# Performance work log

Hardware: AMD Instinct MI355X
Metric: run time of the kernel (lower is better)

The kernel has to match this reference:

```python
import jax, jax.numpy as jnp
import numpy as np

N_NODES = 50000
N_EDGES = 500000
HIDDEN = 128
HEADS = 8
HEAD_DIM = HIDDEN // HEADS


def setup_inputs() -> dict:
    key = jax.random.key(0)
    ks = jax.random.split(key, 20)

    def lin_w(k, fin, fout):
        return (jax.random.normal(k, (fin, fout), jnp.float32) / np.sqrt(fin)).astype(jnp.float32)

    inp = {
        "h": jax.random.normal(ks[0], (N_NODES, HIDDEN), jnp.float32),
        "x": jax.random.normal(ks[1], (N_NODES, 3), jnp.float32),
        "src": jax.random.randint(ks[2], (N_EDGES,), 0, N_NODES, jnp.int32),
        "dst": jax.random.randint(ks[3], (N_EDGES,), 0, N_NODES, jnp.int32),
        "distances": jax.random.uniform(ks[4], (N_EDGES,), jnp.float32),
        # linear layers stored as [in, out] (transposed vs torch nn.Linear)
        "Wq": lin_w(ks[5], HIDDEN, HIDDEN), "bq": jnp.zeros((HIDDEN,), jnp.float32),
        "Wk": lin_w(ks[6], HIDDEN, HIDDEN), "bk": jnp.zeros((HIDDEN,), jnp.float32),
        "Wv": lin_w(ks[7], HIDDEN, HIDDEN), "bv": jnp.zeros((HIDDEN,), jnp.float32),
        "Wo": lin_w(ks[8], HIDDEN, HIDDEN), "bo": jnp.zeros((HIDDEN,), jnp.float32),
        "Wd": lin_w(ks[9], 1, HEADS), "bd": jnp.zeros((HEADS,), jnp.float32),
        "Wg1": lin_w(ks[10], HIDDEN, HIDDEN), "bg1": jnp.zeros((HIDDEN,), jnp.float32),
        "Wg2": lin_w(ks[11], HIDDEN, 1), "bg2": jnp.zeros((1,), jnp.float32),
    }
    return inp


def reference(h, x, src, dst, distances,
              Wq, bq, Wk, bk, Wv, bv, Wo, bo, Wd, bd, Wg1, bg1, Wg2, bg2):
    n = h.shape[0]
    heads = Wd.shape[1]
    dh = Wq.shape[1] // heads

    q = (h @ Wq + bq).reshape(n, heads, dh)
    k = (h @ Wk + bk).reshape(n, heads, dh)
    v = (h @ Wv + bv).reshape(n, heads, dh)

    q_src = q[src]            # [E, heads, dh]
    k_dst = k[dst]
    v_dst = v[dst]

    logits = jnp.einsum('ehd,ehd->eh', q_src, k_dst) / jnp.sqrt(jnp.asarray(dh, h.dtype))
    bias = (distances * distances)[:, None] @ Wd + bd      # [E, heads]
    lg = logits - bias

    # segment softmax over edges grouped by src node
    m = jax.ops.segment_max(lg, src, num_segments=n)        # [N, heads]
    ex = jnp.exp(lg - m[src])
    s = jax.ops.segment_sum(ex, src, num_segments=n)
    w = ex / jnp.maximum(s[src], 1e-9)                      # [E, heads]

    h_upd = jax.ops.segment_sum(v_dst * w[:, :, None], src, num_segments=n)
    h_out = h + h_upd.reshape(n, heads * dh) @ Wo + bo

    w_mean = w.mean(axis=1)                                 # mean over heads -> [E]
    disp = jax.ops.segment_sum((x[dst] - x[src]) * w_mean[:, None], src, num_segments=n)

    gate = jnp.tanh(jax.nn.silu(h_out @ Wg1 + bg1) @ Wg2 + bg2)  # [N, 1]
    x_out = x + gate * disp
    return (h_out, x_out)
```

## Files before the change

### kernel.cpp

```cpp
#include <hip/hip_runtime.h>
#include <math.h>

#define N_NODES 50000
#define N_EDGES 500000
#define HIDDEN 128
#define HEADS 8
#define HEAD_DIM 16

typedef __attribute__((ext_vector_type(8))) short short8;
typedef __attribute__((ext_vector_type(4))) float floatx4;

#define OFF_Q       0u
#define OFF_KV      6400000u
#define OFF_HHI     12800000u
#define OFF_HLO     16000000u
#define OFF_DISP    19200000u
#define OFF_CNT     19350016u
#define OFF_ROWPTR  19400032u
#define OFF_CURSOR  19450048u
#define OFF_ESD     19500064u
#define OFF_WSPLIT  20500064u

static __device__ __forceinline__ unsigned short f2bf(float f) {
    unsigned u = __builtin_bit_cast(unsigned, f);
    unsigned r = (u + 0x7FFFu + ((u >> 16) & 1u)) >> 16;
    return (unsigned short)r;
}
static __device__ __forceinline__ float bf2f(unsigned short s) {
    return __builtin_bit_cast(float, (unsigned)s << 16);
}

__global__ void k_zero_int(int* __restrict__ p, int n) {
    int i = blockIdx.x * 256 + threadIdx.x;
    if (i < n) p[i] = 0;
}

__global__ void k_split_w(const float* __restrict__ Wq, const float* __restrict__ Wk,
                          const float* __restrict__ Wv, const float* __restrict__ Wo,
                          const float* __restrict__ Wg1, unsigned short* __restrict__ ws) {
    int t = blockIdx.x * 256 + threadIdx.x;
    int m = t >> 14, r = t & 16383;
    int k = r >> 7, n = r & 127;
    const float* W = (m == 0) ? Wq : (m == 1) ? Wk : (m == 2) ? Wv : (m == 3) ? Wo : Wg1;
    float x = W[k * 128 + n];
    int kc = k >> 5, kin = k & 31, quad = kin >> 3, j = kin & 7;
    int ct = n >> 4, nin = n & 15, lane = quad * 16 + nin;
    unsigned base = ((((unsigned)(m * 4 + kc) * 8 + ct) * 2) * 64 + lane) * 8 + j;
    unsigned short a = f2bf(x);
    ws[base] = a;
    ws[base + 512] = f2bf(x - bf2f(a));
}

__global__ __launch_bounds__(256) void k_qkv_mfma(
    const float* __restrict__ h, const unsigned short* __restrict__ wsp,
    const float* __restrict__ bq, const float* __restrict__ bk, const float* __restrict__ bv,
    float* __restrict__ q, unsigned* __restrict__ kvp) {
    const int wave = threadIdx.x >> 6, lane = threadIdx.x & 63;
    const int quad = lane >> 4, l15 = lane & 15;
    const int ct0 = wave * 2;
    const int row0 = blockIdx.x * 32;

    floatx4 acc[3][2][2];
#pragma unroll
    for (int m = 0; m < 3; ++m)
#pragma unroll
        for (int c = 0; c < 2; ++c)
#pragma unroll
            for (int r = 0; r < 2; ++r) acc[m][c][r] = (floatx4){0.f, 0.f, 0.f, 0.f};

#pragma unroll
    for (int kc = 0; kc < 4; ++kc) {
        short8 ah[2], al[2];
#pragma unroll
        for (int rt = 0; rt < 2; ++rt) {
            int row = row0 + rt * 16 + l15;
            if (row >= N_NODES) row = N_NODES - 1;
            const float* hp = h + (size_t)row * 128 + kc * 32 + quad * 8;
            float4 f0 = *(const float4*)(hp);
            float4 f1 = *(const float4*)(hp + 4);
            float fv[8] = {f0.x, f0.y, f0.z, f0.w, f1.x, f1.y, f1.z, f1.w};
#pragma unroll
            for (int j = 0; j < 8; ++j) {
                unsigned short hi = f2bf(fv[j]);
                ah[rt][j] = (short)hi;
                al[rt][j] = (short)f2bf(fv[j] - bf2f(hi));
            }
        }
#pragma unroll
        for (int m = 0; m < 3; ++m) {
#pragma unroll
            for (int ctl = 0; ctl < 2; ++ctl) {
                unsigned fb = ((((unsigned)(m * 4 + kc) * 8 + (ct0 + ctl)) * 2) * 64 + lane) * 8;
                short8 bh = *(const short8*)(wsp + fb);
                short8 bl = *(const short8*)(wsp + fb + 512);
#pragma unroll
                for (int rt = 0; rt < 2; ++rt) {
                    acc[m][ctl][rt] = __builtin_amdgcn_mfma_f32_16x16x32_bf16(
                        ah[rt], bh, acc[m][ctl][rt], 0, 0, 0);
                    acc[m][ctl][rt] = __builtin_amdgcn_mfma_f32_16x16x32_bf16(
                        ah[rt], bl, acc[m][ctl][rt], 0, 0, 0);
                    acc[m][ctl][rt] = __builtin_amdgcn_mfma_f32_16x16x32_bf16(
                        al[rt], bh, acc[m][ctl][rt], 0, 0, 0);
                }
            }
        }
    }

#pragma unroll
    for (int ctl = 0; ctl < 2; ++ctl) {
        int col = (ct0 + ctl) * 16 + l15;
        float bq_ = bq[col], bk_ = bk[col], bv_ = bv[col];
#pragma unroll
        for (int rt = 0; rt < 2; ++rt) {
#pragma unroll
            for (int reg = 0; reg < 4; ++reg) {
                int row = row0 + rt * 16 + quad * 4 + reg;
                if (row < N_NODES) {
                    q[(size_t)row * 128 + col] = acc[0][ctl][rt][reg] + bq_;
                    unsigned kb = f2bf(acc[1][ctl][rt][reg] + bk_);
                    unsigned vb = f2bf(acc[2][ctl][rt][reg] + bv_);
                    kvp[(size_t)row * 128 + col] = kb | (vb << 16);
                }
            }
        }
    }
}

__global__ void k_count(const int* __restrict__ src, int* __restrict__ cnt) {
    int e = blockIdx.x * 256 + threadIdx.x;
    if (e < N_EDGES) atomicAdd(&cnt[src[e]], 1);
}

__global__ __launch_bounds__(1024) void k_scan1(const int* __restrict__ cnt,
                                                int* __restrict__ loc,
                                                int* __restrict__ bsum, int n) {
    __shared__ int buf[1024];
    int t = threadIdx.x;
    int i = blockIdx.x * 1024 + t;
    int val = (i < n) ? cnt[i] : 0;
    buf[t] = val;
    __syncthreads();
    for (int off = 1; off < 1024; off <<= 1) {
        int a = (t >= off) ? buf[t - off] : 0;
        __syncthreads();
        buf[t] += a;
        __syncthreads();
    }
    if (i < n) loc[i] = buf[t];
    if (t == 1023) bsum[blockIdx.x] = buf[1023];
}

__global__ void k_scan2(int* __restrict__ bsum, int nb) {
    int t = threadIdx.x;
    int v = (t < nb) ? bsum[t] : 0;
    for (int off = 1; off < 64; off <<= 1) {
        int a = __shfl_up(v, off);
        if (t >= off) v += a;
    }
    if (t < nb) bsum[t] = v;
}

__global__ void k_scan3(const int* __restrict__ cnt, const int* __restrict__ loc,
                        const int* __restrict__ bsum,
                        int* __restrict__ rowptr, int* __restrict__ cursor, int n) {
    int i = blockIdx.x * 256 + threadIdx.x;
    if (i < n) {
        int off = (i >= 1024) ? bsum[(i >> 10) - 1] : 0;
        int incl = loc[i] + off;
        rowptr[i + 1] = incl;
        cursor[i] = incl - cnt[i];
    }
    if (i == 0) rowptr[0] = 0;
}

__global__ void k_scatter(const int* __restrict__ src, const int* __restrict__ dst,
                          const float* __restrict__ dist, int* __restrict__ cursor,
                          int2* __restrict__ esd) {
    int e = blockIdx.x * 256 + threadIdx.x;
    if (e < N_EDGES) {
        int pos = atomicAdd(&cursor[src[e]], 1);
        float dd = dist[e];
        esd[pos] = make_int2(dst[e], __float_as_int(dd * dd));
    }
}

__global__ __launch_bounds__(256) void k_edge_node(
    const float* __restrict__ q, const unsigned* __restrict__ kvp,
    const float* __restrict__ x,
    const int2* __restrict__ esd, const int* __restrict__ rowptr,
    const float* __restrict__ Wd, const float* __restrict__ bd,
    unsigned short* __restrict__ hupd_hi, unsigned short* __restrict__ hupd_lo,
    float* __restrict__ disp) {
    const int wave = threadIdx.x >> 6, lane = threadIdx.x & 63;
    const int node = blockIdx.x * 4 + wave;
    const int h = lane >> 3, sub = lane & 7;
    const int beg = rowptr[node], end = rowptr[node + 1];

    const float2 qv = *(const float2*)(q + (size_t)node * 128 + 2 * lane);
    const float wdh = Wd[h], bdh = bd[h];
    const bool dal = (sub < 3);
    float xs = dal ? x[node * 3 + sub] : 0.f;
    const unsigned colo = 2 * lane;

    float acc0 = 0.f, acc1 = 0.f, s_own = 0.f, da = 0.f;

    for (int cb = beg; cb < end; cb += 64) {
        int idx = cb + lane;
        int dvec = 0; float d2vec = 0.f;
        if (idx < end) {
            int2 ed = esd[idx];
            dvec = ed.x;
            d2vec = __int_as_float(ed.y);
        }
        int clen = min(64, end - cb);
        int i = 0;
        for (; i + 4 <= clen; i += 4) {
            int di[4]; float dd2[4]; uint2 kv2[4]; float xg[4];
#pragma unroll
            for (int j = 0; j < 4; ++j) {
                di[j]  = __shfl(dvec, i + j);
                dd2[j] = __shfl(d2vec, i + j);
            }
#pragma unroll
            for (int j = 0; j < 4; ++j)
                kv2[j] = *(const uint2*)(kvp + (unsigned)di[j] * 128u + colo);
#pragma unroll
            for (int j = 0; j < 4; ++j)
                xg[j] = dal ? x[(unsigned)di[j] * 3u + sub] : 0.f;
#pragma unroll
            for (int j = 0; j < 4; ++j) {
                float k0 = __builtin_bit_cast(float, kv2[j].x << 16);
                float v0 = __builtin_bit_cast(float, kv2[j].x & 0xFFFF0000u);
                float k1 = __builtin_bit_cast(float, kv2[j].y << 16);
                float v1 = __builtin_bit_cast(float, kv2[j].y & 0xFFFF0000u);
                float p = qv.x * k0 + qv.y * k1;
                p += __shfl_xor(p, 1);
                p += __shfl_xor(p, 2);
                p += __shfl_xor(p, 4);
                float w = __expf(p * 0.25f - (dd2[j] * wdh + bdh));
                s_own += w;
                acc0 += v0 * w;
                acc1 += v1 * w;
                da += (xg[j] - xs) * w;
            }
        }
        for (; i < clen; ++i) {
            int dij  = __shfl(dvec, i);
            float d2 = __shfl(d2vec, i);
            uint2 kv2 = *(const uint2*)(kvp + (unsigned)dij * 128u + colo);
            float xgj = dal ? x[(unsigned)dij * 3u + sub] : 0.f;
            float k0 = __builtin_bit_cast(float, kv2.x << 16);
            float v0 = __builtin_bit_cast(float, kv2.x & 0xFFFF0000u);
            float k1 = __builtin_bit_cast(float, kv2.y << 16);
            float v1 = __builtin_bit_cast(float, kv2.y & 0xFFFF0000u);
            float p = qv.x * k0 + qv.y * k1;
            p += __shfl_xor(p, 1);
            p += __shfl_xor(p, 2);
            p += __shfl_xor(p, 4);
            float w = __expf(p * 0.25f - (d2 * wdh + bdh));
            s_own += w;
            acc0 += v0 * w;
            acc1 += v1 * w;
            da += (xgj - xs) * w;
        }
    }

    float inva = 1.f / fmaxf(s_own, 1e-9f);
    float o0 = acc0 * inva, o1 = acc1 * inva;
    unsigned short h0 = f2bf(o0), h1 = f2bf(o1);
    unsigned short l0 = f2bf(o0 - bf2f(h0)), l1 = f2bf(o1 - bf2f(h1));
    ((unsigned*)hupd_hi)[(size_t)node * 64 + lane] = (unsigned)h0 | ((unsigned)h1 << 16);
    ((unsigned*)hupd_lo)[(size_t)node * 64 + lane] = (unsigned)l0 | ((unsigned)l1 << 16);

    da *= 0.125f * inva;
    da += __shfl_xor(da, 8);
    da += __shfl_xor(da, 16);
    da += __shfl_xor(da, 32);
    if (lane < 3) disp[node * 3 + lane] = da;
}

__global__ __launch_bounds__(256) void k_hout_gate(
    const float* __restrict__ h,
    const unsigned short* __restrict__ hupd_hi, const unsigned short* __restrict__ hupd_lo,
    const unsigned short* __restrict__ wsp,
    const float* __restrict__ bo, const float* __restrict__ bg1,
    const float* __restrict__ Wg2, const float* __restrict__ bg2,
    const float* __restrict__ x, const float* __restrict__ disp,
    float* __restrict__ hout, float* __restrict__ xout) {
    __shared__ float hb[4][16 * 132];
    const int wave = threadIdx.x >> 6, lane = threadIdx.x & 63;
    const int quad = lane >> 4, l15 = lane & 15;
    const int row0 = blockIdx.x * 64 + wave * 16;
    float* hbw = hb[wave];

    floatx4 acc[8];
#pragma unroll
    for (int c = 0; c < 8; ++c) acc[c] = (floatx4){0.f, 0.f, 0.f, 0.f};
#pragma unroll
    for (int kc = 0; kc < 4; ++kc) {
        int row = row0 + l15;
        if (row >= N_NODES) row = N_NODES - 1;
        size_t aoff = (size_t)row * 128 + kc * 32 + quad * 8;
        short8 ah = *(const short8*)(hupd_hi + aoff);
        short8 al = *(const short8*)(hupd_lo + aoff);
#pragma unroll
        for (int ct = 0; ct < 8; ++ct) {
            unsigned fb = ((((unsigned)(3 * 4 + kc) * 8 + ct) * 2) * 64 + lane) * 8;
            short8 bh = *(const short8*)(wsp + fb);
            short8 bl = *(const short8*)(wsp + fb + 512);
            acc[ct] = __builtin_amdgcn_mfma_f32_16x16x32_bf16(ah, bh, acc[ct], 0, 0, 0);
            acc[ct] = __builtin_amdgcn_mfma_f32_16x16x32_bf16(ah, bl, acc[ct], 0, 0, 0);
            acc[ct] = __builtin_amdgcn_mfma_f32_16x16x32_bf16(al, bh, acc[ct], 0, 0, 0);
        }
    }

#pragma unroll
    for (int ct = 0; ct < 8; ++ct) {
        int col = ct * 16 + l15;
        float bias = bo[col];
#pragma unroll
        for (int reg = 0; reg < 4; ++reg) {
            int row = row0 + quad * 4 + reg;
            float val = acc[ct][reg] + bias;
            if (row < N_NODES) {
                val += h[(size_t)row * 128 + col];
                hout[(size_t)row * 128 + col] = val;
            }
            hbw[(quad * 4 + reg) * 132 + col] = val;
        }
    }
    __asm__ volatile("s_waitcnt lgkmcnt(0)" ::: "memory");

    floatx4 acc2[8];
#pragma unroll
    for (int c = 0; c < 8; ++c) acc2[c] = (floatx4){0.f, 0.f, 0.f, 0.f};
#pragma unroll
    for (int kc = 0; kc < 4; ++kc) {
        const float* ap = hbw + l15 * 132 + kc * 32 + quad * 8;
        float4 f0 = *(const float4*)(ap);
        float4 f1 = *(const float4*)(ap + 4);
        float fv[8] = {f0.x, f0.y, f0.z, f0.w, f1.x, f1.y, f1.z, f1.w};
        short8 ah, al;
#pragma unroll
        for (int j = 0; j < 8; ++j) {
            unsigned short hi = f2bf(fv[j]);
            ah[j] = (short)hi;
            al[j] = (short)f2bf(fv[j] - bf2f(hi));
        }
#pragma unroll
        for (int ct = 0; ct < 8; ++ct) {
            unsigned fb = ((((unsigned)(4 * 4 + kc) * 8 + ct) * 2) * 64 + lane) * 8;
            short8 bh = *(const short8*)(wsp + fb);
            short8 bl = *(const short8*)(wsp + fb + 512);
            acc2[ct] = __builtin_amdgcn_mfma_f32_16x16x32_bf16(ah, bh, acc2[ct], 0, 0, 0);
            acc2[ct] = __builtin_amdgcn_mfma_f32_16x16x32_bf16(ah, bl, acc2[ct], 0, 0, 0);
            acc2[ct] = __builtin_amdgcn_mfma_f32_16x16x32_bf16(al, bh, acc2[ct], 0, 0, 0);
        }
    }

    float pr[4] = {0.f, 0.f, 0.f, 0.f};
#pragma unroll
    for (int ct = 0; ct < 8; ++ct) {
        int col = ct * 16 + l15;
        float b1 = bg1[col];
        float w2 = Wg2[col];
#pragma unroll
        for (int reg = 0; reg < 4; ++reg) {
            float z = acc2[ct][reg] + b1;
            pr[reg] += (z / (1.f + __expf(-z))) * w2;
        }
    }
#pragma unroll
    for (int off = 1; off < 16; off <<= 1) {
#pragma unroll
        for (int reg = 0; reg < 4; ++reg) pr[reg] += __shfl_xor(pr[reg], off);
    }
    if (l15 == 0) {
        float b2 = bg2[0];
#pragma unroll
        for (int reg = 0; reg < 4; ++reg) {
            int row = row0 + quad * 4 + reg;
            if (row < N_NODES) {
                float g = tanhf(pr[reg] + b2);
#pragma unroll
                for (int dd = 0; dd < 3; ++dd) {
                    int oo = row * 3 + dd;
                    xout[oo] = x[oo] + g * disp[oo];
                }
            }
        }
    }
}

extern "C" void kernel_launch(void* const* d_in, const int* in_sizes, int n_in,
                              void* d_out, int out_size, void* d_ws, size_t ws_size,
                              hipStream_t stream) {
    const float* h    = (const float*)d_in[0];
    const float* x    = (const float*)d_in[1];
    const int*   src  = (const int*)d_in[2];
    const int*   dst  = (const int*)d_in[3];
    const float* dist = (const float*)d_in[4];
    const float* Wq = (const float*)d_in[5];  const float* bq = (const float*)d_in[6];
    const float* Wk = (const float*)d_in[7];  const float* bk = (const float*)d_in[8];
    const float* Wv = (const float*)d_in[9];  const float* bv = (const float*)d_in[10];
    const float* Wo = (const float*)d_in[11]; const float* bo = (const float*)d_in[12];
    const float* Wd = (const float*)d_in[13]; const float* bd = (const float*)d_in[14];
    const float* Wg1 = (const float*)d_in[15]; const float* bg1 = (const float*)d_in[16];
    const float* Wg2 = (const float*)d_in[17]; const float* bg2 = (const float*)d_in[18];

    float* ws    = (float*)d_ws;
    float* q     = ws + OFF_Q;
    unsigned* kvp = (unsigned*)(ws + OFF_KV);
    float* disp  = ws + OFF_DISP;
    int* cnt     = (int*)(ws + OFF_CNT);
    int* rowptr  = (int*)(ws + OFF_ROWPTR);
    int* cursor  = (int*)(ws + OFF_CURSOR);
    int2* esd    = (int2*)(ws + OFF_ESD);
    unsigned short* wsp = (unsigned short*)(ws + OFF_WSPLIT);
    int* loc    = (int*)(ws + OFF_Q);
    int* bsum   = (int*)(ws + OFF_Q + 500000u);
    unsigned short* hupd_hi = (unsigned short*)(ws + OFF_HHI);
    unsigned short* hupd_lo = (unsigned short*)(ws + OFF_HLO);
    float* hout = (float*)d_out;
    float* xout = hout + (size_t)N_NODES * HIDDEN;

    const int nscan = (N_NODES + 1023) / 1024;

    k_split_w<<<320, 256, 0, stream>>>(Wq, Wk, Wv, Wo, Wg1, wsp);
    k_zero_int<<<(N_NODES + 255) / 256, 256, 0, stream>>>(cnt, N_NODES);
    k_count<<<(N_EDGES + 255) / 256, 256, 0, stream>>>(src, cnt);
    k_scan1<<<nscan, 1024, 0, stream>>>(cnt, loc, bsum, N_NODES);
    k_scan2<<<1, 64, 0, stream>>>(bsum, nscan);
    k_scan3<<<(N_NODES + 255) / 256, 256, 0, stream>>>(cnt, loc, bsum, rowptr, cursor, N_NODES);
    k_scatter<<<(N_EDGES + 255) / 256, 256, 0, stream>>>(src, dst, dist, cursor, esd);
    k_qkv_mfma<<<(N_NODES + 31) / 32, 256, 0, stream>>>(h, wsp, bq, bk, bv, q, kvp);
    k_edge_node<<<N_NODES / 4, 256, 0, stream>>>(q, kvp, x, esd, rowptr,
                                                 Wd, bd, hupd_hi, hupd_lo, disp);
    k_hout_gate<<<(N_NODES + 63) / 64, 256, 0, stream>>>(h, hupd_hi, hupd_lo, wsp,
                                                         bo, bg1, Wg2, bg2,
                                                         x, disp, hout, xout);
}
```

Before: 286.9 us.

## Merge small preprocessing kernels and co-launch QKV GEMM with edge scatter

Folds the weight split and count zeroing into one launch, merges the two scan fix-up kernels into one that redoes the tiny block-sum scan per block in shared memory, and packs the QKV MFMA GEMM and the CSR edge scatter into a single grid whose block ranges do different work. This cuts the kernel launch count from nine to six and lets the compute-bound GEMM blocks overlap with the atomic-bound scatter blocks. The cost is a heterogeneous grid, where the GEMM blocks' register use sets occupancy for the scatter blocks, plus redundant scan work in every scan23 block.

New measurement: 262.7 us. 1.09x faster.

```diff
diff --git a/kernel.cpp b/kernel.cpp
--- a/kernel.cpp
+++ b/kernel.cpp
@@ -6,6 +6,11 @@
 #define HIDDEN 128
 #define HEADS 8
 #define HEAD_DIM 16
+
+#define QKV_BLOCKS 1563
+#define SCAT_BLOCKS 1954
+#define SPLITW_BLOCKS 320
+#define ZERO_BLOCKS 196
 
 typedef __attribute__((ext_vector_type(8))) short short8;
 typedef __attribute__((ext_vector_type(4))) float floatx4;
@@ -30,14 +35,15 @@
     return __builtin_bit_cast(float, (unsigned)s << 16);
 }
 
-__global__ void k_zero_int(int* __restrict__ p, int n) {
-    int i = blockIdx.x * 256 + threadIdx.x;
-    if (i < n) p[i] = 0;
-}
-
-__global__ void k_split_w(const float* __restrict__ Wq, const float* __restrict__ Wk,
-                          const float* __restrict__ Wv, const float* __restrict__ Wo,
-                          const float* __restrict__ Wg1, unsigned short* __restrict__ ws) {
+__global__ void k_prep(const float* __restrict__ Wq, const float* __restrict__ Wk,
+                       const float* __restrict__ Wv, const float* __restrict__ Wo,
+                       const float* __restrict__ Wg1, unsigned short* __restrict__ ws,
+                       int* __restrict__ cnt) {
+    if (blockIdx.x >= SPLITW_BLOCKS) {
+        int i = (blockIdx.x - SPLITW_BLOCKS) * 256 + threadIdx.x;
+        if (i < N_NODES) cnt[i] = 0;
+        return;
+    }
     int t = blockIdx.x * 256 + threadIdx.x;
     int m = t >> 14, r = t & 16383;
     int k = r >> 7, n = r & 127;
@@ -49,81 +55,6 @@
     unsigned short a = f2bf(x);
     ws[base] = a;
     ws[base + 512] = f2bf(x - bf2f(a));
-}
-
-__global__ __launch_bounds__(256) void k_qkv_mfma(
-    const float* __restrict__ h, const unsigned short* __restrict__ wsp,
-    const float* __restrict__ bq, const float* __restrict__ bk, const float* __restrict__ bv,
-    float* __restrict__ q, unsigned* __restrict__ kvp) {
-    const int wave = threadIdx.x >> 6, lane = threadIdx.x & 63;
-    const int quad = lane >> 4, l15 = lane & 15;
-    const int ct0 = wave * 2;
-    const int row0 = blockIdx.x * 32;
-
-    floatx4 acc[3][2][2];
-#pragma unroll
-    for (int m = 0; m < 3; ++m)
-#pragma unroll
-        for (int c = 0; c < 2; ++c)
-#pragma unroll
-            for (int r = 0; r < 2; ++r) acc[m][c][r] = (floatx4){0.f, 0.f, 0.f, 0.f};
-
-#pragma unroll
-    for (int kc = 0; kc < 4; ++kc) {
-        short8 ah[2], al[2];
-#pragma unroll
-        for (int rt = 0; rt < 2; ++rt) {
-            int row = row0 + rt * 16 + l15;
-            if (row >= N_NODES) row = N_NODES - 1;
-            const float* hp = h + (size_t)row * 128 + kc * 32 + quad * 8;
-            float4 f0 = *(const float4*)(hp);
-            float4 f1 = *(const float4*)(hp + 4);
-            float fv[8] = {f0.x, f0.y, f0.z, f0.w, f1.x, f1.y, f1.z, f1.w};
-#pragma unroll
-            for (int j = 0; j < 8; ++j) {
-                unsigned short hi = f2bf(fv[j]);
-                ah[rt][j] = (short)hi;
-                al[rt][j] = (short)f2bf(fv[j] - bf2f(hi));
-            }
-        }
-#pragma unroll
-        for (int m = 0; m < 3; ++m) {
-#pragma unroll
-            for (int ctl = 0; ctl < 2; ++ctl) {
-                unsigned fb = ((((unsigned)(m * 4 + kc) * 8 + (ct0 + ctl)) * 2) * 64 + lane) * 8;
-                short8 bh = *(const short8*)(wsp + fb);
-                short8 bl = *(const short8*)(wsp + fb + 512);
-#pragma unroll
-                for (int rt = 0; rt < 2; ++rt) {
-                    acc[m][ctl][rt] = __builtin_amdgcn_mfma_f32_16x16x32_bf16(
-                        ah[rt], bh, acc[m][ctl][rt], 0, 0, 0);
-                    acc[m][ctl][rt] = __builtin_amdgcn_mfma_f32_16x16x32_bf16(
-                        ah[rt], bl, acc[m][ctl][rt], 0, 0, 0);
-                    acc[m][ctl][rt] = __builtin_amdgcn_mfma_f32_16x16x32_bf16(
-                        al[rt], bh, acc[m][ctl][rt], 0, 0, 0);
-                }
-            }
-        }
-    }
-
-#pragma unroll
-    for (int ctl = 0; ctl < 2; ++ctl) {
-        int col = (ct0 + ctl) * 16 + l15;
-        float bq_ = bq[col], bk_ = bk[col], bv_ = bv[col];
-#pragma unroll
-        for (int rt = 0; rt < 2; ++rt) {
-#pragma unroll
-            for (int reg = 0; reg < 4; ++reg) {
-                int row = row0 + rt * 16 + quad * 4 + reg;
-                if (row < N_NODES) {
-                    q[(size_t)row * 128 + col] = acc[0][ctl][rt][reg] + bq_;
-                    unsigned kb = f2bf(acc[1][ctl][rt][reg] + bk_);
-                    unsigned vb = f2bf(acc[2][ctl][rt][reg] + bv_);
-                    kvp[(size_t)row * 128 + col] = kb | (vb << 16);
-                }
-            }
-        }
-    }
 }
 
 __global__ void k_count(const int* __restrict__ src, int* __restrict__ cnt) {
@@ -150,22 +81,25 @@
     if (t == 1023) bsum[blockIdx.x] = buf[1023];
 }
 
-__global__ void k_scan2(int* __restrict__ bsum, int nb) {
+__global__ __launch_bounds__(256) void k_scan23(const int* __restrict__ cnt,
+                                                const int* __restrict__ loc,
+                                                const int* __restrict__ bsum,
+                                                int* __restrict__ rowptr,
+                                                int* __restrict__ cursor, int n, int nb) {
+    __shared__ int sb[64];
     int t = threadIdx.x;
-    int v = (t < nb) ? bsum[t] : 0;
-    for (int off = 1; off < 64; off <<= 1) {
-        int a = __shfl_up(v, off);
-        if (t >= off) v += a;
-    }
-    if (t < nb) bsum[t] = v;
-}
-
-__global__ void k_scan3(const int* __restrict__ cnt, const int* __restrict__ loc,
-                        const int* __restrict__ bsum,
-                        int* __restrict__ rowptr, int* __restrict__ cursor, int n) {
-    int i = blockIdx.x * 256 + threadIdx.x;
+    if (t < 64) {
+        int v = (t < nb) ? bsum[t] : 0;
+        for (int off = 1; off < 64; off <<= 1) {
+            int a = __shfl_up(v, off);
+            if (t >= off) v += a;
+        }
+        sb[t] = v;
+    }
+    __syncthreads();
+    int i = blockIdx.x * 256 + t;
     if (i < n) {
-        int off = (i >= 1024) ? bsum[(i >> 10) - 1] : 0;
+        int off = (i >= 1024) ? sb[(i >> 10) - 1] : 0;
         int incl = loc[i] + off;
         rowptr[i + 1] = incl;
         cursor[i] = incl - cnt[i];
@@ -173,14 +107,90 @@
     if (i == 0) rowptr[0] = 0;
 }
 
-__global__ void k_scatter(const int* __restrict__ src, const int* __restrict__ dst,
-                          const float* __restrict__ dist, int* __restrict__ cursor,
-                          int2* __restrict__ esd) {
-    int e = blockIdx.x * 256 + threadIdx.x;
-    if (e < N_EDGES) {
-        int pos = atomicAdd(&cursor[src[e]], 1);
-        float dd = dist[e];
-        esd[pos] = make_int2(dst[e], __float_as_int(dd * dd));
+__global__ __launch_bounds__(256) void k_qkv_scatter(
+    const float* __restrict__ h, const unsigned short* __restrict__ wsp,
+    const float* __restrict__ bq, const float* __restrict__ bk, const float* __restrict__ bv,
+    float* __restrict__ q, unsigned* __restrict__ kvp,
+    const int* __restrict__ src, const int* __restrict__ dst,
+    const float* __restrict__ dist, int* __restrict__ cursor, int2* __restrict__ esd) {
+    if (blockIdx.x >= QKV_BLOCKS) {
+        int e = (blockIdx.x - QKV_BLOCKS) * 256 + threadIdx.x;
+        if (e < N_EDGES) {
+            int pos = atomicAdd(&cursor[src[e]], 1);
+            float dd = dist[e];
+            esd[pos] = make_int2(dst[e], __float_as_int(dd * dd));
+        }
+        return;
+    }
+
+    const int wave = threadIdx.x >> 6, lane = threadIdx.x & 63;
+    const int quad = lane >> 4, l15 = lane & 15;
+    const int ct0 = wave * 2;
+    const int row0 = blockIdx.x * 32;
+
+    floatx4 acc[3][2][2];
+#pragma unroll
+    for (int m = 0; m < 3; ++m)
+#pragma unroll
+        for (int c = 0; c < 2; ++c)
+#pragma unroll
+            for (int r = 0; r < 2; ++r) acc[m][c][r] = (floatx4){0.f, 0.f, 0.f, 0.f};
+
+#pragma unroll
+    for (int kc = 0; kc < 4; ++kc) {
+        short8 ah[2], al[2];
+#pragma unroll
+        for (int rt = 0; rt < 2; ++rt) {
+            int row = row0 + rt * 16 + l15;
+            if (row >= N_NODES) row = N_NODES - 1;
+            const float* hp = h + (size_t)row * 128 + kc * 32 + quad * 8;
+            float4 f0 = *(const float4*)(hp);
+            float4 f1 = *(const float4*)(hp + 4);
+            float fv[8] = {f0.x, f0.y, f0.z, f0.w, f1.x, f1.y, f1.z, f1.w};
+#pragma unroll
+            for (int j = 0; j < 8; ++j) {
+                unsigned short hi = f2bf(fv[j]);
+                ah[rt][j] = (short)hi;
+                al[rt][j] = (short)f2bf(fv[j] - bf2f(hi));
+            }
+        }
+#pragma unroll
+        for (int m = 0; m < 3; ++m) {
+#pragma unroll
+            for (int ctl = 0; ctl < 2; ++ctl) {
+                unsigned fb = ((((unsigned)(m * 4 + kc) * 8 + (ct0 + ctl)) * 2) * 64 + lane) * 8;
+                short8 bh = *(const short8*)(wsp + fb);
+                short8 bl = *(const short8*)(wsp + fb + 512);
+#pragma unroll
+                for (int rt = 0; rt < 2; ++rt) {
+                    acc[m][ctl][rt] = __builtin_amdgcn_mfma_f32_16x16x32_bf16(
+                        ah[rt], bh, acc[m][ctl][rt], 0, 0, 0);
+                    acc[m][ctl][rt] = __builtin_amdgcn_mfma_f32_16x16x32_bf16(
+                        ah[rt], bl, acc[m][ctl][rt], 0, 0, 0);
+                    acc[m][ctl][rt] = __builtin_amdgcn_mfma_f32_16x16x32_bf16(
+                        al[rt], bh, acc[m][ctl][rt], 0, 0, 0);
+                }
+            }
+        }
+    }
+
+#pragma unroll
+    for (int ctl = 0; ctl < 2; ++ctl) {
+        int col = (ct0 + ctl) * 16 + l15;
+        float bq_ = bq[col], bk_ = bk[col], bv_ = bv[col];
+#pragma unroll
+        for (int rt = 0; rt < 2; ++rt) {
+#pragma unroll
+            for (int reg = 0; reg < 4; ++reg) {
+                int row = row0 + rt * 16 + quad * 4 + reg;
+                if (row < N_NODES) {
+                    q[(size_t)row * 128 + col] = acc[0][ctl][rt][reg] + bq_;
+                    unsigned kb = f2bf(acc[1][ctl][rt][reg] + bk_);
+                    unsigned vb = f2bf(acc[2][ctl][rt][reg] + bv_);
+                    kvp[(size_t)row * 128 + col] = kb | (vb << 16);
+                }
+            }
+        }
     }
 }
 
@@ -426,14 +436,12 @@
 
     const int nscan = (N_NODES + 1023) / 1024;
 
-    k_split_w<<<320, 256, 0, stream>>>(Wq, Wk, Wv, Wo, Wg1, wsp);
-    k_zero_int<<<(N_NODES + 255) / 256, 256, 0, stream>>>(cnt, N_NODES);
-    k_count<<<(N_EDGES + 255) / 256, 256, 0, stream>>>(src, cnt);
+    k_prep<<<SPLITW_BLOCKS + ZERO_BLOCKS, 256, 0, stream>>>(Wq, Wk, Wv, Wo, Wg1, wsp, cnt);
+    k_count<<<SCAT_BLOCKS, 256, 0, stream>>>(src, cnt);
     k_scan1<<<nscan, 1024, 0, stream>>>(cnt, loc, bsum, N_NODES);
-    k_scan2<<<1, 64, 0, stream>>>(bsum, nscan);
-    k_scan3<<<(N_NODES + 255) / 256, 256, 0, stream>>>(cnt, loc, bsum, rowptr, cursor, N_NODES);
-    k_scatter<<<(N_EDGES + 255) / 256, 256, 0, stream>>>(src, dst, dist, cursor, esd);
-    k_qkv_mfma<<<(N_NODES + 31) / 32, 256, 0, stream>>>(h, wsp, bq, bk, bv, q, kvp);
+    k_scan23<<<ZERO_BLOCKS, 256, 0, stream>>>(cnt, loc, bsum, rowptr, cursor, N_NODES, nscan);
+    k_qkv_scatter<<<QKV_BLOCKS + SCAT_BLOCKS, 256, 0, stream>>>(
+        h, wsp, bq, bk, bv, q, kvp, src, dst, dist, cursor, esd);
     k_edge_node<<<N_NODES / 4, 256, 0, stream>>>(q, kvp, x, esd, rowptr,
                                                  Wd, bd, hupd_hi, hupd_lo, disp);
     k_hout_gate<<<(N_NODES + 63) / 64, 256, 0, stream>>>(h, hupd_hi, hupd_lo, wsp,
```
